# Optimization experiments

Hardware: AMD Instinct MI355X
Metric: run time of the kernel (lower is better)

Reference implementation:

```python
import jax, jax.numpy as jnp
import numpy as np

K = 3            # kernel_size
S = 4            # up_factor
VMAX = 1.0
TAU = 0.5
CENTER_BIAS = 2.5
SMOOTH_RES = 0.15
C_IN = 21
HIDDEN = 48
B_, H0, W0 = 4, 81, 81
CTR = K // 2      # = 1, also GL recursion depth M


def _dir_step_diff(k):
    """Precompute (base_pos - base_neg) per direction/step: [8, M+1, k, k]."""
    c = k // 2
    dirs = np.array([[1, 0], [1, 1], [0, 1], [-1, 1], [-1, 0], [-1, -1], [0, -1], [1, -1]], np.float32)
    dirs = dirs / (np.linalg.norm(dirs, axis=1, keepdims=True) + 1e-8)
    yy, xx = np.meshgrid(np.arange(k), np.arange(k), indexing='ij')
    rel = np.stack([yy - c, xx - c], -1).astype(np.float32)
    diff = np.zeros((8, c + 1, k, k), np.float32)
    for d in range(8):
        v = dirs[d]
        proj = rel[..., 0] * v[1] + rel[..., 1] * v[0]
        step = np.clip(np.round(proj), -c, c).astype(np.int64)
        for m in range(c + 1):
            diff[d, m] = (step == m).astype(np.float32) - (step == -m).astype(np.float32)
    return diff

DIFF = jnp.asarray(_dir_step_diff(K))  # [8, M+1, K, K]


def conv3x3(x, w, b):
    y = jax.lax.conv_general_dilated(x, w, (1, 1), 'SAME',
                                     dimension_numbers=('NCHW', 'OIHW', 'NCHW'))
    return y + b[None, :, None, None]


def bilinear_up(x, s):
    """F.interpolate(scale_factor=s, mode='bilinear', align_corners=True)."""
    B, C, h, w = x.shape
    H, W = h * s, w * s
    ys = jnp.linspace(0.0, h - 1.0, H)
    xs = jnp.linspace(0.0, w - 1.0, W)
    y0 = jnp.clip(jnp.floor(ys).astype(jnp.int32), 0, h - 2)
    x0 = jnp.clip(jnp.floor(xs).astype(jnp.int32), 0, w - 2)
    wy = (ys - y0)[:, None]
    wx = (xs - x0)[None, :]
    x00 = x[:, :, y0][:, :, :, x0]
    x01 = x[:, :, y0][:, :, :, x0 + 1]
    x10 = x[:, :, y0 + 1][:, :, :, x0]
    x11 = x[:, :, y0 + 1][:, :, :, x0 + 1]
    return (x00 * (1 - wy) * (1 - wx) + x01 * (1 - wy) * wx
            + x10 * wy * (1 - wx) + x11 * wy * wx)


def setup_inputs() -> dict:
    key = jax.random.key(0)
    ks = jax.random.split(key, 6)
    wn = lambda k, shape: jax.random.normal(k, shape, jnp.float32) * 0.05
    return {
        'x': jax.random.normal(ks[0], (B_, C_IN, H0, W0), jnp.float32),
        'w1o': wn(ks[1], (HIDDEN, C_IN, 3, 3)), 'b1o': jnp.zeros((HIDDEN,), jnp.float32),
        'w2o': wn(ks[2], (8, HIDDEN, 3, 3)), 'b2o': jnp.zeros((8,), jnp.float32),
        'w1g': wn(ks[3], (HIDDEN, C_IN, 3, 3)), 'b1g': jnp.zeros((HIDDEN,), jnp.float32),
        'w2g': wn(ks[4], (1, HIDDEN, 3, 3)), 'b2g': jnp.zeros((1,), jnp.float32),
        'beta': jnp.asarray(1.6, jnp.float32),
    }


def reference(x, w1o, b1o, w2o, b2o, w1g, b1g, w2g, b2g, beta):
    B, C, h, w = x.shape
    c = CTR
    # heads
    raw_v = conv3x3(jax.nn.relu(conv3x3(x, w1o, b1o)), w2o, b2o)          # [B,8,h,w]
    g = jax.nn.sigmoid(conv3x3(jax.nn.relu(conv3x3(x, w1g, b1g)), w2g, b2g))  # [B,1,h,w]
    v = VMAX * jnp.tanh(raw_v)
    # Gruenwald-Letnikov coefficients, M = center (=1 for k=3)
    coeffs = [jnp.ones_like(v)]
    wm = coeffs[0]
    for m in range(1, c + 1):
        wm = wm * (v - m + 1.0) / m * -1.0
        coeffs.append(wm)
    coeff = jnp.stack(coeffs, axis=2)                                      # [B,8,M+1,h,w]
    # direction kernels, averaged over the 8 directions
    ker = jnp.einsum('bdmhw,dmkl->bklhw', coeff, DIFF) / 8.0               # [B,K,K,h,w]
    mask_pre = ker.reshape(B, K * K, h, w)
    ci = c * K + c
    # NOTE: torch adds center_bias in-place on a view of ker -> ker itself is biased too
    mask_pre = mask_pre.at[:, ci].add(CENTER_BIAS)
    ker_b = mask_pre.reshape(B, K, K, h, w)
    mask_lp = jax.nn.softmax(mask_pre / TAU, axis=1)                       # [B,9,h,w]
    # unfold 3x3 window with reflect padding
    xp = jnp.pad(x, ((0, 0), (0, 0), (c, c), (c, c)), mode='reflect')
    patches = jnp.stack([xp[:, :, i:i + h, j:j + w]
                         for i in range(K) for j in range(K)], axis=2)     # [B,C,9,h,w]
    rep2 = lambda a, ax: jnp.repeat(jnp.repeat(a, S, axis=ax), S, axis=ax + 1)
    neigh = rep2(patches, 3)                                               # [B,C,9,H,W]
    mask_lp_u = rep2(mask_lp, 2)                                           # [B,9,H,W]
    g_up = rep2(g, 2)                                                      # [B,1,H,W]
    x_up = bilinear_up(x, S)                                               # [B,C,H,W]
    y_lp_out = jnp.einsum('bcnHW,bnHW->bcHW', neigh, mask_lp_u)
    lam = SMOOTH_RES * (1.0 - g_up)
    y_lp = x_up + lam * (y_lp_out - x_up)
    # highpass branch (mode='both')
    ker_hp = ker_b - ker_b.mean(axis=(1, 2), keepdims=True)
    ker_hp = ker_hp / (jnp.abs(ker_hp).sum(axis=(1, 2), keepdims=True) + 1e-8)
    mask_hp = rep2(ker_hp.reshape(B, K * K, h, w), 2)
    y_hp = jnp.einsum('bcnHW,bnHW->bcHW', neigh, mask_hp)
    y = y_lp + jnp.tanh(beta) * g_up * y_hp
    return (y, v, g_up)
```

## Files before the change

### kernel.cpp

```cpp
#include <hip/hip_runtime.h>
#include <math.h>

#define B_N   4
#define CIN   21
#define HIDC  48
#define H0    81
#define NP    6561
#define HH    324
#define NPH   104976

__device__ __forceinline__ float tanh_fast(float x) {
    float e = __expf(2.f * x);
    return 1.f - 2.f / (e + 1.f);
}

__global__ __launch_bounds__(256) void k1_conv1(
    const float* __restrict__ x,
    const float* __restrict__ w1o, const float* __restrict__ b1o,
    const float* __restrict__ w1g, const float* __restrict__ b1g,
    float* __restrict__ hid_o, float* __restrict__ hid_g)
{
    __shared__ __align__(16) float wt[189 * 12];
    __shared__ float bs[12];
    const int tid = threadIdx.x;
    const int grp = blockIdx.y;
    const int b   = blockIdx.z;
    const bool head_o = (grp < 4);
    const int ocb = (grp & 3) * 12;
    const float* wsrc = head_o ? w1o : w1g;
    for (int i = tid; i < 189 * 12; i += 256) {
        const int ict = i / 12, oc = i - ict * 12;
        wt[i] = wsrc[(ocb + oc) * 189 + ict];
    }
    if (tid < 12) bs[tid] = (head_o ? b1o : b1g)[ocb + tid];
    __syncthreads();

    const int px = blockIdx.x * 256 + tid;
    const bool valid = (px < NP);
    const int oy = px / H0, ox = px - oy * H0;
    const float* xb = x + (size_t)b * CIN * NP;

    float acc[12];
    #pragma unroll
    for (int j = 0; j < 12; j++) acc[j] = bs[j];

    for (int ic = 0; ic < CIN; ic++) {
        const float* xc = xb + ic * NP;
        float xv[9];
        #pragma unroll
        for (int ky = 0; ky < 3; ky++) {
            const int iy = oy + ky - 1;
            const bool rok = valid && ((unsigned)iy < (unsigned)H0);
            #pragma unroll
            for (int kx = 0; kx < 3; kx++) {
                const int ix = ox + kx - 1;
                const bool ok = rok && ((unsigned)ix < (unsigned)H0);
                xv[ky * 3 + kx] = ok ? xc[iy * H0 + ix] : 0.f;
            }
        }
        #pragma unroll
        for (int tap = 0; tap < 9; tap++) {
            const float4 w0 = *(const float4*)&wt[(ic * 9 + tap) * 12];
            const float4 w1 = *(const float4*)&wt[(ic * 9 + tap) * 12 + 4];
            const float4 w2 = *(const float4*)&wt[(ic * 9 + tap) * 12 + 8];
            const float wj[12] = {w0.x, w0.y, w0.z, w0.w, w1.x, w1.y, w1.z, w1.w,
                                  w2.x, w2.y, w2.z, w2.w};
            const float xvt = xv[tap];
            #pragma unroll
            for (int j = 0; j < 12; j++) acc[j] = fmaf(xvt, wj[j], acc[j]);
        }
    }

    if (valid) {
        float* outp = (head_o ? hid_o : hid_g) + ((size_t)b * HIDC + ocb) * NP + px;
        #pragma unroll
        for (int j = 0; j < 12; j++) outp[j * NP] = fmaxf(acc[j], 0.f);
    }
}

__global__ __launch_bounds__(256) void k2up(
    const float* __restrict__ x,
    const float* __restrict__ hid_o, const float* __restrict__ hid_g,
    const float* __restrict__ w2o, const float* __restrict__ b2o,
    const float* __restrict__ w2g, const float* __restrict__ b2g,
    const float* __restrict__ beta,
    float* __restrict__ v_out, float* __restrict__ y_out,
    float* __restrict__ gup_out)
{
    __shared__ __align__(16) float wo_s[HIDC * 9 * 8];
    __shared__ float wg_s[HIDC * 9];
    __shared__ float red[4][32][12];
    __shared__ float res_s[32][29];
    __shared__ float alp2[CIN][32];
    __shared__ float ahp2[CIN][32];
    const int tid = threadIdx.x;
    const int b = blockIdx.y;

    for (int i = tid; i < HIDC * 9 * 8; i += 256) {
        const int d = i / (HIDC * 9), r = i - d * (HIDC * 9);
        wo_s[r * 8 + d] = w2o[i];
    }
    for (int i = tid; i < HIDC * 9; i += 256) wg_s[i] = w2g[i];
    __syncthreads();

    const int pxl = tid & 31;
    const int s   = tid >> 5;
    const int w   = tid >> 6;
    const int px0 = blockIdx.x * 32;
    const int px  = px0 + pxl;
    const bool valid = (px < NP);
    const int oy = px / H0, ox = px - oy * H0;
    const int ic0 = s * 6;
    const float* po = hid_o + ((size_t)b * HIDC + ic0) * NP;
    const float* pg = hid_g + ((size_t)b * HIDC + ic0) * NP;

    float a[8] = {0.f, 0.f, 0.f, 0.f, 0.f, 0.f, 0.f, 0.f};
    float ag = 0.f;

    #pragma unroll 1
    for (int ky = 0; ky < 3; ky++) {
        const int iy = oy + ky - 1;
        const bool rok = valid && ((unsigned)iy < (unsigned)H0);
        #pragma unroll
        for (int kx = 0; kx < 3; kx++) {
            const int ix = ox + kx - 1;
            const bool ok = rok && ((unsigned)ix < (unsigned)H0);
            const int off = iy * H0 + ix;
            const int tap = ky * 3 + kx;
            #pragma unroll
            for (int j = 0; j < 6; j++) {
                const float vo = ok ? po[j * NP + off] : 0.f;
                const float vg = ok ? pg[j * NP + off] : 0.f;
                const int wb = ((ic0 + j) * 9 + tap) * 8;
                const float4 wA = *(const float4*)&wo_s[wb];
                const float4 wB = *(const float4*)&wo_s[wb + 4];
                a[0] = fmaf(vo, wA.x, a[0]); a[1] = fmaf(vo, wA.y, a[1]);
                a[2] = fmaf(vo, wA.z, a[2]); a[3] = fmaf(vo, wA.w, a[3]);
                a[4] = fmaf(vo, wB.x, a[4]); a[5] = fmaf(vo, wB.y, a[5]);
                a[6] = fmaf(vo, wB.z, a[6]); a[7] = fmaf(vo, wB.w, a[7]);
                ag = fmaf(vg, wg_s[(ic0 + j) * 9 + tap], ag);
            }
        }
    }

    #pragma unroll
    for (int n = 0; n < 8; n++) a[n] += __shfl_xor(a[n], 32);
    ag += __shfl_xor(ag, 32);
    if ((tid & 32) == 0) {
        #pragma unroll
        for (int n = 0; n < 8; n++) red[w][pxl][n] = a[n];
        red[w][pxl][8] = ag;
    }
    __syncthreads();

    if (tid < 32 && valid) {
        float v[8];
        #pragma unroll
        for (int n = 0; n < 8; n++)
            v[n] = tanh_fast(red[0][tid][n] + red[1][tid][n] + red[2][tid][n]
                             + red[3][tid][n] + b2o[n]);
        const float agf = red[0][tid][8] + red[1][tid][8] + red[2][tid][8]
                        + red[3][tid][8] + b2g[0];
        const float g = 1.f / (1.f + __expf(-agf));

        constexpr float DT[8][9] = {
            {-1, 0, 1, -1, 0, 1, -1, 0, 1},
            {-1,-1, 0, -1, 0, 1,  0, 1, 1},
            {-1,-1,-1,  0, 0, 0,  1, 1, 1},
            { 0,-1,-1,  1, 0,-1,  1, 1, 0},
            { 1, 0,-1,  1, 0,-1,  1, 0,-1},
            { 1, 1, 0,  1, 0,-1,  0,-1,-1},
            { 1, 1, 1,  0, 0, 0, -1,-1,-1},
            { 0, 1, 1, -1, 0, 1, -1,-1, 0}};
        float ker[9];
        #pragma unroll
        for (int n = 0; n < 9; n++) {
            float t = 0.f;
            #pragma unroll
            for (int d = 0; d < 8; d++) t += v[d] * DT[d][n];
            ker[n] = -0.125f * t;
        }
        ker[4] += 2.5f;
        float mx = ker[0];
        #pragma unroll
        for (int n = 1; n < 9; n++) mx = fmaxf(mx, ker[n]);
        float exn[9], sum = 0.f;
        #pragma unroll
        for (int n = 0; n < 9; n++) { exn[n] = __expf((ker[n] - mx) * 2.0f); sum += exn[n]; }
        const float rs = 1.f / sum;
        float mean = 0.f;
        #pragma unroll
        for (int n = 0; n < 9; n++) mean += ker[n];
        mean *= (1.f / 9.f);
        float den = 1e-8f;
        #pragma unroll
        for (int n = 0; n < 9; n++) den += fabsf(ker[n] - mean);
        const float rd = 1.f / den;

        #pragma unroll
        for (int n = 0; n < 8; n++) res_s[tid][n] = v[n];
        res_s[tid][8] = g;
        #pragma unroll
        for (int n = 0; n < 9; n++) {
            res_s[tid][9 + n]  = exn[n] * rs;
            res_s[tid][18 + n] = (ker[n] - mean) * rd;
        }
    }
    __syncthreads();

    {
        const int plane = tid >> 5, pl = tid & 31;
        const int p = px0 + pl;
        if (p < NP) v_out[((size_t)b * 8 + plane) * NP + p] = res_s[pl][plane];
    }

    for (int i = tid; i < CIN * 32; i += 256) {
        const int c = i >> 5, pl = i & 31;
        const int p = px0 + pl;
        if (p >= NP) continue;
        const int py = p / H0, pxc = p - py * H0;
        const int ym = (py == 0) ? 1 : py - 1;
        const int yp = (py == H0 - 1) ? H0 - 2 : py + 1;
        const int xm = (pxc == 0) ? 1 : pxc - 1;
        const int xp = (pxc == H0 - 1) ? H0 - 2 : pxc + 1;
        const float* xc = x + ((size_t)b * CIN + c) * NP;
        const int ry[3] = {ym, py, yp};
        const int rx[3] = {xm, pxc, xp};
        float alp = 0.f, ahp = 0.f;
        #pragma unroll
        for (int t = 0; t < 3; t++) {
            const float* xr = xc + ry[t] * H0;
            #pragma unroll
            for (int u = 0; u < 3; u++) {
                const float xv = xr[rx[u]];
                alp = fmaf(xv, res_s[pl][9 + t * 3 + u], alp);
                ahp = fmaf(xv, res_s[pl][18 + t * 3 + u], ahp);
            }
        }
        alp2[c][pl] = alp;
        ahp2[c][pl] = ahp;
    }
    __syncthreads();

    const float tb = tanh_fast(beta[0]);
    for (int i = tid; i < 22 * 4 * 32; i += 256) {
        const int pl  = i >> 7;
        const int rem = i & 127;
        const int dh  = rem >> 5, pp = rem & 31;
        const int p = px0 + pp;
        if (p >= NP) continue;
        const int py = p / H0, pxc = p - py * H0;
        const int H = py * 4 + dh;
        const float g = res_s[pp][8];
        if (pl == 21) {
            *reinterpret_cast<float4*>(gup_out + (size_t)b * NPH + H * HH + pxc * 4) =
                make_float4(g, g, g, g);
            continue;
        }
        const int c = pl;
        const float lam = 0.15f * (1.f - g);
        const float gh = tb * g;
        const float alp = alp2[c][pp];
        const float ahp = ahp2[c][pp];
        const float ysf = (float)H * (80.f / 323.f);
        int y0 = (int)ysf;
        if (y0 > H0 - 2) y0 = H0 - 2;
        const float wy = ysf - (float)y0;
        const float* xc = x + ((size_t)b * CIN + c) * NP;
        const int cm = (pxc == 0) ? 0 : pxc - 1;
        const int cp = (pxc == H0 - 1) ? H0 - 1 : pxc + 1;
        const float a0 = xc[y0 * H0 + cm];
        const float a1 = xc[y0 * H0 + pxc];
        const float a2 = xc[y0 * H0 + cp];
        const float b0 = xc[(y0 + 1) * H0 + cm];
        const float b1 = xc[(y0 + 1) * H0 + pxc];
        const float b2 = xc[(y0 + 1) * H0 + cp];
        float res[4];
        #pragma unroll
        for (int k = 0; k < 4; k++) {
            const int W = pxc * 4 + k;
            const float xsf = (float)W * (80.f / 323.f);
            int x0 = (int)xsf;
            if (x0 > H0 - 2) x0 = H0 - 2;
            const float wx = xsf - (float)x0;
            const int sx = x0 - pxc + 1;
            const float top = (sx == 0) ? fmaf(a1 - a0, wx, a0) : fmaf(a2 - a1, wx, a1);
            const float bot = (sx == 0) ? fmaf(b1 - b0, wx, b0) : fmaf(b2 - b1, wx, b1);
            const float xup = fmaf(bot - top, wy, top);
            res[k] = fmaf(lam, alp - xup, xup) + gh * ahp;
        }
        *reinterpret_cast<float4*>(y_out + ((size_t)b * CIN + c) * NPH + H * HH + pxc * 4) =
            make_float4(res[0], res[1], res[2], res[3]);
    }
}

extern "C" void kernel_launch(void* const* d_in, const int* in_sizes, int n_in,
                              void* d_out, int out_size, void* d_ws, size_t ws_size,
                              hipStream_t stream)
{
    const float* x    = (const float*)d_in[0];
    const float* w1o  = (const float*)d_in[1];
    const float* b1o  = (const float*)d_in[2];
    const float* w2o  = (const float*)d_in[3];
    const float* b2o  = (const float*)d_in[4];
    const float* w1g  = (const float*)d_in[5];
    const float* b1g  = (const float*)d_in[6];
    const float* w2g  = (const float*)d_in[7];
    const float* b2g  = (const float*)d_in[8];
    const float* beta = (const float*)d_in[9];
    float* out = (float*)d_out;
    float* wsf = (float*)d_ws;

    float* hid_o = wsf;
    float* hid_g = hid_o + (size_t)B_N * HIDC * NP;

    float* y_out = out;
    float* v_out = out + (size_t)B_N * CIN * NPH;
    float* gup   = v_out + (size_t)B_N * 8 * NP;

    k1_conv1<<<dim3((NP + 255) / 256, 8, B_N), 256, 0, stream>>>(
        x, w1o, b1o, w1g, b1g, hid_o, hid_g);
    k2up<<<dim3((NP + 31) / 32, B_N), 256, 0, stream>>>(
        x, hid_o, hid_g, w2o, b2o, w2g, b2g, beta, v_out, y_out, gup);
}
```

Measured before the change: 146.1 us.

## Prefetch x 3x3 windows into registers and fuse lowpass/highpass with upsample output

```diff
diff --git a/kernel.cpp b/kernel.cpp
--- a/kernel.cpp
+++ b/kernel.cpp
@@ -78,7 +78,7 @@
     }
 }
 
-__global__ __launch_bounds__(256) void k2up(
+__global__ __launch_bounds__(256, 3) void k2up(
     const float* __restrict__ x,
     const float* __restrict__ hid_o, const float* __restrict__ hid_g,
     const float* __restrict__ w2o, const float* __restrict__ b2o,
@@ -91,10 +91,45 @@
     __shared__ float wg_s[HIDC * 9];
     __shared__ float red[4][32][12];
     __shared__ float res_s[32][29];
-    __shared__ float alp2[CIN][32];
-    __shared__ float ahp2[CIN][32];
     const int tid = threadIdx.x;
     const int b = blockIdx.y;
+
+    const int pl  = tid & 31;
+    const int s   = tid >> 5;
+    const int w   = tid >> 6;
+    const int px0 = blockIdx.x * 32;
+    const int px  = px0 + pl;
+    const bool valid = (px < NP);
+    const int py  = px / H0, pxc = px - py * H0;
+
+    float xw0[9], xw1[9], xw2[9];
+    {
+        const int ym = (py == 0) ? 1 : py - 1;
+        const int yp = (py == H0 - 1) ? H0 - 2 : py + 1;
+        const int xm = (pxc == 0) ? 1 : pxc - 1;
+        const int xp = (pxc == H0 - 1) ? H0 - 2 : pxc + 1;
+        const int ro[3] = {ym * H0, py * H0, yp * H0};
+        const int co[3] = {xm, pxc, xp};
+        if (valid) {
+            const float* xb0 = x + ((size_t)b * CIN + s) * NP;
+            const float* xb1 = xb0 + 8 * NP;
+            #pragma unroll
+            for (int t = 0; t < 3; t++)
+                #pragma unroll
+                for (int u = 0; u < 3; u++) {
+                    xw0[t * 3 + u] = xb0[ro[t] + co[u]];
+                    xw1[t * 3 + u] = xb1[ro[t] + co[u]];
+                }
+            if (s < 5) {
+                const float* xb2 = xb0 + 16 * NP;
+                #pragma unroll
+                for (int t = 0; t < 3; t++)
+                    #pragma unroll
+                    for (int u = 0; u < 3; u++)
+                        xw2[t * 3 + u] = xb2[ro[t] + co[u]];
+            }
+        }
+    }
 
     for (int i = tid; i < HIDC * 9 * 8; i += 256) {
         const int d = i / (HIDC * 9), r = i - d * (HIDC * 9);
@@ -103,13 +138,6 @@
     for (int i = tid; i < HIDC * 9; i += 256) wg_s[i] = w2g[i];
     __syncthreads();
 
-    const int pxl = tid & 31;
-    const int s   = tid >> 5;
-    const int w   = tid >> 6;
-    const int px0 = blockIdx.x * 32;
-    const int px  = px0 + pxl;
-    const bool valid = (px < NP);
-    const int oy = px / H0, ox = px - oy * H0;
     const int ic0 = s * 6;
     const float* po = hid_o + ((size_t)b * HIDC + ic0) * NP;
     const float* pg = hid_g + ((size_t)b * HIDC + ic0) * NP;
@@ -119,11 +147,11 @@
 
     #pragma unroll 1
     for (int ky = 0; ky < 3; ky++) {
-        const int iy = oy + ky - 1;
+        const int iy = py + ky - 1;
         const bool rok = valid && ((unsigned)iy < (unsigned)H0);
         #pragma unroll
         for (int kx = 0; kx < 3; kx++) {
-            const int ix = ox + kx - 1;
+            const int ix = pxc + kx - 1;
             const bool ok = rok && ((unsigned)ix < (unsigned)H0);
             const int off = iy * H0 + ix;
             const int tap = ky * 3 + kx;
@@ -148,8 +176,8 @@
     ag += __shfl_xor(ag, 32);
     if ((tid & 32) == 0) {
         #pragma unroll
-        for (int n = 0; n < 8; n++) red[w][pxl][n] = a[n];
-        red[w][pxl][8] = ag;
+        for (int n = 0; n < 8; n++) red[w][pl][n] = a[n];
+        red[w][pl][8] = ag;
     }
     __syncthreads();
 
@@ -208,89 +236,82 @@
     }
     __syncthreads();
 
-    {
-        const int plane = tid >> 5, pl = tid & 31;
-        const int p = px0 + pl;
-        if (p < NP) v_out[((size_t)b * 8 + plane) * NP + p] = res_s[pl][plane];
-    }
-
-    for (int i = tid; i < CIN * 32; i += 256) {
-        const int c = i >> 5, pl = i & 31;
-        const int p = px0 + pl;
-        if (p >= NP) continue;
-        const int py = p / H0, pxc = p - py * H0;
-        const int ym = (py == 0) ? 1 : py - 1;
-        const int yp = (py == H0 - 1) ? H0 - 2 : py + 1;
-        const int xm = (pxc == 0) ? 1 : pxc - 1;
-        const int xp = (pxc == H0 - 1) ? H0 - 2 : pxc + 1;
-        const float* xc = x + ((size_t)b * CIN + c) * NP;
-        const int ry[3] = {ym, py, yp};
-        const int rx[3] = {xm, pxc, xp};
-        float alp = 0.f, ahp = 0.f;
-        #pragma unroll
-        for (int t = 0; t < 3; t++) {
-            const float* xr = xc + ry[t] * H0;
-            #pragma unroll
-            for (int u = 0; u < 3; u++) {
-                const float xv = xr[rx[u]];
-                alp = fmaf(xv, res_s[pl][9 + t * 3 + u], alp);
-                ahp = fmaf(xv, res_s[pl][18 + t * 3 + u], ahp);
-            }
-        }
-        alp2[c][pl] = alp;
-        ahp2[c][pl] = ahp;
-    }
-    __syncthreads();
-
-    const float tb = tanh_fast(beta[0]);
-    for (int i = tid; i < 22 * 4 * 32; i += 256) {
-        const int pl  = i >> 7;
-        const int rem = i & 127;
-        const int dh  = rem >> 5, pp = rem & 31;
-        const int p = px0 + pp;
-        if (p >= NP) continue;
-        const int py = p / H0, pxc = p - py * H0;
-        const int H = py * 4 + dh;
-        const float g = res_s[pp][8];
-        if (pl == 21) {
-            *reinterpret_cast<float4*>(gup_out + (size_t)b * NPH + H * HH + pxc * 4) =
-                make_float4(g, g, g, g);
-            continue;
-        }
-        const int c = pl;
-        const float lam = 0.15f * (1.f - g);
-        const float gh = tb * g;
-        const float alp = alp2[c][pp];
-        const float ahp = ahp2[c][pp];
-        const float ysf = (float)H * (80.f / 323.f);
-        int y0 = (int)ysf;
-        if (y0 > H0 - 2) y0 = H0 - 2;
-        const float wy = ysf - (float)y0;
-        const float* xc = x + ((size_t)b * CIN + c) * NP;
-        const int cm = (pxc == 0) ? 0 : pxc - 1;
-        const int cp = (pxc == H0 - 1) ? H0 - 1 : pxc + 1;
-        const float a0 = xc[y0 * H0 + cm];
-        const float a1 = xc[y0 * H0 + pxc];
-        const float a2 = xc[y0 * H0 + cp];
-        const float b0 = xc[(y0 + 1) * H0 + cm];
-        const float b1 = xc[(y0 + 1) * H0 + pxc];
-        const float b2 = xc[(y0 + 1) * H0 + cp];
-        float res[4];
+    if (px0 + pl < NP) v_out[((size_t)b * 8 + s) * NP + px0 + pl] = res_s[pl][s];
+
+    if (valid) {
+        const float tb  = tanh_fast(beta[0]);
+        const float gv  = res_s[pl][8];
+        const float lam = 0.15f * (1.f - gv);
+        const float gh  = tb * gv;
+
+        int syv[4]; float wyv[4];
+        #pragma unroll
+        for (int dh = 0; dh < 4; dh++) {
+            const int H = py * 4 + dh;
+            const float ysf = (float)H * (80.f / 323.f);
+            int y0 = (int)ysf;
+            if (y0 > H0 - 2) y0 = H0 - 2;
+            wyv[dh] = ysf - (float)y0;
+            syv[dh] = y0 - py + 1;
+        }
+        int sxv[4]; float wxv[4];
         #pragma unroll
         for (int k = 0; k < 4; k++) {
             const int W = pxc * 4 + k;
             const float xsf = (float)W * (80.f / 323.f);
             int x0 = (int)xsf;
             if (x0 > H0 - 2) x0 = H0 - 2;
-            const float wx = xsf - (float)x0;
-            const int sx = x0 - pxc + 1;
-            const float top = (sx == 0) ? fmaf(a1 - a0, wx, a0) : fmaf(a2 - a1, wx, a1);
-            const float bot = (sx == 0) ? fmaf(b1 - b0, wx, b0) : fmaf(b2 - b1, wx, b1);
-            const float xup = fmaf(bot - top, wy, top);
-            res[k] = fmaf(lam, alp - xup, xup) + gh * ahp;
-        }
-        *reinterpret_cast<float4*>(y_out + ((size_t)b * CIN + c) * NPH + H * HH + pxc * 4) =
-            make_float4(res[0], res[1], res[2], res[3]);
+            wxv[k] = xsf - (float)x0;
+            sxv[k] = x0 - pxc + 1;
+        }
+
+#define EMIT_PLANE(CC, XW) do {                                              \
+        float alp = 0.f, ahp = 0.f;                                          \
+        _Pragma("unroll")                                                    \
+        for (int t = 0; t < 9; t++) {                                        \
+            alp = fmaf(XW[t], res_s[pl][9 + t],  alp);                       \
+            ahp = fmaf(XW[t], res_s[pl][18 + t], ahp);                       \
+        }                                                                    \
+        float* ydst = y_out + ((size_t)b * CIN + (CC)) * NPH;                \
+        _Pragma("unroll")                                                    \
+        for (int dh = 0; dh < 4; dh++) {                                     \
+            const int sy = syv[dh];                                          \
+            const float wy = wyv[dh];                                        \
+            const float A0 = sy ? XW[3] : XW[0];                             \
+            const float A1 = sy ? XW[4] : XW[1];                             \
+            const float A2 = sy ? XW[5] : XW[2];                             \
+            const float B0 = sy ? XW[6] : XW[3];                             \
+            const float B1 = sy ? XW[7] : XW[4];                             \
+            const float B2 = sy ? XW[8] : XW[5];                             \
+            float rr[4];                                                     \
+            _Pragma("unroll")                                                \
+            for (int k = 0; k < 4; k++) {                                    \
+                const float wx = wxv[k];                                     \
+                const float top = sxv[k] ? fmaf(A2 - A1, wx, A1)             \
+                                         : fmaf(A1 - A0, wx, A0);            \
+                const float bot = sxv[k] ? fmaf(B2 - B1, wx, B1)             \
+                                         : fmaf(B1 - B0, wx, B0);            \
+                const float xup = fmaf(bot - top, wy, top);                  \
+                rr[k] = fmaf(lam, alp - xup, xup) + gh * ahp;                \
+            }                                                                \
+            *reinterpret_cast<float4*>(ydst + (size_t)(py * 4 + dh) * HH     \
+                                       + pxc * 4) =                          \
+                make_float4(rr[0], rr[1], rr[2], rr[3]);                     \
+        }                                                                    \
+    } while (0)
+
+        EMIT_PLANE(s,     xw0);
+        EMIT_PLANE(s + 8, xw1);
+        if (s < 5) {
+            EMIT_PLANE(s + 16, xw2);
+        } else if (s == 5) {
+            float* gdst = gup_out + (size_t)b * NPH;
+            #pragma unroll
+            for (int dh = 0; dh < 4; dh++)
+                *reinterpret_cast<float4*>(gdst + (size_t)(py * 4 + dh) * HH + pxc * 4) =
+                    make_float4(gv, gv, gv, gv);
+        }
+#undef EMIT_PLANE
     }
 }
 
```

Measured after the change: 201.2 us. +37.7%, slower.
